# Optimization experiments

Measured on AMD Instinct MI355X. Metric: run time of the kernel, lower is better.

The kernel has to match this reference:

```python
import jax, jax.numpy as jnp
import numpy as np

Z1, COND, HID, NSTEP, B = 128, 12, 1024, 32, 4096


def setup_inputs() -> dict:
    key = jax.random.key(0)
    ks = jax.random.split(key, 10)
    s = 0.05  # init scale for learned params
    return {
        "z": jax.random.normal(ks[0], (B, Z1), jnp.float32),
        "condition": jax.random.uniform(ks[1], (B, NSTEP, COND), jnp.float32),
        "iteration": 1000,
        # nn.GRUCell params (gate order: r, z, n)
        "W_ih": jax.random.normal(ks[2], (3 * HID, Z1 + COND), jnp.float32) * s,
        "W_hh": jax.random.normal(ks[3], (3 * HID, HID), jnp.float32) * s,
        "b_ih": jax.random.normal(ks[4], (3 * HID,), jnp.float32) * s,
        "b_hh": jax.random.normal(ks[5], (3 * HID,), jnp.float32) * s,
        # linear_init_0
        "W_init": jax.random.normal(ks[6], (HID, Z1), jnp.float32) * s,
        "b_init": jax.random.normal(ks[7], (HID,), jnp.float32) * s,
        # linear_out_0
        "W_out": jax.random.normal(ks[8], (COND, HID), jnp.float32) * s,
        "b_out": jax.random.normal(ks[9], (COND,), jnp.float32) * s,
    }


def reference(z, condition, iteration, W_ih, W_hh, b_ih, b_hh, W_init, b_init, W_out, b_out):
    # Deterministic teacher-forcing path (training, eps=1): feedback at step i
    # is zeros for i=0, else condition[:, i-1, :]. iteration only affects the
    # stochastic eps schedule, which is dropped for determinism.
    del iteration
    b = z.shape[0]
    hx = jnp.tanh(z @ W_init.T + b_init)  # [B, H]
    feed = jnp.concatenate(
        [jnp.zeros((b, 1, COND), z.dtype), condition[:, :-1, :]], axis=1)  # [B, T, C]
    inputs = jnp.concatenate(
        [feed, jnp.broadcast_to(z[:, None, :], (b, NSTEP, z.shape[1]))], axis=-1)
    # precompute all input-to-hidden projections, time-major: [T, B, 3H]
    gi = jnp.einsum('bti,gi->tbg', inputs, W_ih) + b_ih

    def step(h, gi_t):
        gh = h @ W_hh.T + b_hh
        i_r, i_z, i_n = jnp.split(gi_t, 3, axis=-1)
        h_r, h_z, h_n = jnp.split(gh, 3, axis=-1)
        r = jax.nn.sigmoid(i_r + h_r)
        u = jax.nn.sigmoid(i_z + h_z)
        n = jnp.tanh(i_n + r * h_n)
        h_new = (1.0 - u) * n + u * h
        x = jax.nn.sigmoid(h_new @ W_out.T + b_out)  # [B, C]
        return h_new, x

    _, xs = jax.lax.scan(step, hx, gi)  # xs: [T, B, C]
    return jnp.transpose(xs, (1, 0, 2))  # [B, T, C]
```

## Files before the change

kernel.cpp:

```cpp
#include <hip/hip_runtime.h>
#include <stdint.h>

#define BB    4096
#define Z1D   128
#define CD    12
#define HD    1024
#define TT    32
#define N3H   3072
#define KAUG  1184
#define NGP   3168
#define NPH0B 1088
#define ACOLS 160

typedef __bf16 bf16;
typedef __bf16 bf16x2 __attribute__((ext_vector_type(2)));
typedef __bf16 bf16x8 __attribute__((ext_vector_type(8)));
typedef float  f32x4  __attribute__((ext_vector_type(4)));
typedef float  f4     __attribute__((ext_vector_type(4)));

typedef const __attribute__((address_space(1))) void* as1cv;
typedef __attribute__((address_space(3))) void* as3v;

__device__ __forceinline__ float sigm(float x){ return 1.0f/(1.0f+__expf(-x)); }
__device__ __forceinline__ float tanhfast(float x){ return 1.0f - 2.0f/(1.0f+__expf(2.0f*x)); }

__device__ __forceinline__ int rowOfN(int np, int& g){
  int jb = np/96; int r = np - jb*96; g = r>>5; int jl = r&31;
  return g*1024 + jb*32 + jl;
}

__global__ __launch_bounds__(256)
void prep_k(const float* __restrict__ z, const float* __restrict__ Wih,
            const float* __restrict__ Whh, const float* __restrict__ bih,
            const float* __restrict__ bhh, const float* __restrict__ Winit,
            const float* __restrict__ Wout,
            bf16* __restrict__ Wg, bf16* __restrict__ Wzn, bf16* __restrict__ Wi0,
            bf16* __restrict__ zbf, float* __restrict__ biasz,
            float* __restrict__ bhhn, float* __restrict__ bihn,
            bf16* __restrict__ A0, bf16* __restrict__ A1)
{
  const int N1 = NGP*KAUG;
  const int N2 = NPH0B*Z1D;
  const int N3 = NPH0B*Z1D;
  const int N4 = BB*Z1D;
  const int N5 = N3H;
  const int N6 = HD;
  const int N6b= HD;
  const int N7 = 2*BB*ACOLS;
  int idx = blockIdx.x*256 + threadIdx.x;
  if (idx < N1){
    int np = idx/KAUG, k = idx - np*KAUG;
    float v = 0.0f;
    if (np < N3H){
      int g; int row = rowOfN(np, g);
      if (k < 1024) v = Whh[(size_t)row*HD + k];
      else if (g < 2){
        if (k < 1036)      v = Wih[(size_t)row*140 + (k-1024)];
        else if (k < 1164) v = Wih[(size_t)row*140 + 12 + (k-1036)];
      }
    } else {
      int c = np - N3H;
      if (c < CD && k < 1024) v = Wout[(size_t)c*HD + k];
    }
    Wg[idx] = (bf16)v;
    return;
  }
  idx -= N1;
  if (idx < N2){
    int jn = idx/Z1D, kk = idx - jn*Z1D;
    Wzn[idx] = (jn < HD) ? (bf16)Wih[(size_t)(2048+jn)*140 + 12 + kk] : (bf16)0.0f;
    return;
  }
  idx -= N2;
  if (idx < N3){
    int jn = idx/Z1D, kk = idx - jn*Z1D;
    Wi0[idx] = (jn < HD) ? (bf16)Winit[(size_t)jn*Z1D + kk] : (bf16)0.0f;
    return;
  }
  idx -= N3;
  if (idx < N4){ zbf[idx] = (bf16)z[idx]; return; }
  idx -= N4;
  if (idx < N5){
    int g; int row = rowOfN(idx, g);
    biasz[idx] = (g < 2) ? (bih[row] + bhh[row]) : 0.0f;
    return;
  }
  idx -= N5;
  if (idx < N6){ bhhn[idx] = bhh[2048 + idx]; return; }
  idx -= N6;
  if (idx < N6b){ bihn[idx] = bih[2048 + idx]; return; }
  idx -= N6b;
  if (idx < N7){
    int j = (idx < BB*ACOLS) ? idx : idx - BB*ACOLS;
    int b = j / ACOLS, kk = j - b*ACOLS;
    int k = 1024 + kk;
    bf16 v = (bf16)0.0f;
    if (k >= 1036 && k < 1164) v = (bf16)z[(size_t)b*Z1D + (k-1036)];
    if (idx < BB*ACOLS) A0[(size_t)b*KAUG + k] = v;
    else                A1[(size_t)b*KAUG + k] = v;
  }
}

template<int EP>
__global__ __launch_bounds__(256, 5)
void gemm_k(const bf16* __restrict__ A, int lda,
            const bf16* __restrict__ Bw, int ldb, int ksteps,
            const bf16* __restrict__ zpn, bf16* __restrict__ zpnw,
            const float* __restrict__ biasz, const float* __restrict__ bias1,
            const float* __restrict__ bhhn,
            const float* __restrict__ Wih, const float* __restrict__ cond,
            const bf16* __restrict__ Acur, bf16* __restrict__ Anext,
            const float* __restrict__ bout, float* __restrict__ outg, int t)
{
  __shared__ bf16 lA[2][128*32];
  __shared__ bf16 lB[2][96*32];
  const int tid = threadIdx.x, wid = tid>>6, lane = tid&63;
  const int l15 = lane&15, l4 = lane>>4;

  int bx, by;
  if constexpr (EP == 2){
    int bid = blockIdx.x;
    int x = bid & 7, k = bid >> 3;
    bx = k >> 2;
    by = x*4 + (k & 3);
  } else {
    bx = blockIdx.x; by = blockIdx.y;
  }
  const int n0 = bx*96, m0 = by*128;

  f32x4 acc[2][6];
  #pragma unroll
  for (int i=0;i<2;++i)
    #pragma unroll
    for (int j=0;j<6;++j) acc[i][j] = (f32x4){0.f,0.f,0.f,0.f};

  auto STAGE = [&](int buf, int ks){
    const int k0 = ks*32;
    const bf16* gA = A + (size_t)m0*lda + k0;
    #pragma unroll
    for (int r=0; r<2; ++r){
      int q = r*256 + tid;
      int row = q>>2, slot = q&3;
      int sg = slot ^ ((row>>1)&3);
      const bf16* gp = gA + (size_t)row*lda + sg*8;
      bf16* lp = &lA[buf][(size_t)(r*256 + wid*64)*8];
      __builtin_amdgcn_global_load_lds((as1cv)gp, (as3v)lp, 16, 0, 0);
    }
    const bf16* gB = Bw + (size_t)n0*ldb + k0;
    {
      int q = tid;
      int row = q>>2, slot = q&3;
      int sg = slot ^ ((row>>1)&3);
      const bf16* gp = gB + (size_t)row*ldb + sg*8;
      bf16* lp = &lB[buf][(size_t)(wid*64)*8];
      __builtin_amdgcn_global_load_lds((as1cv)gp, (as3v)lp, 16, 0, 0);
    }
    if (tid < 128){
      int q = 256 + tid;
      int row = q>>2, slot = q&3;
      int sg = slot ^ ((row>>1)&3);
      const bf16* gp = gB + (size_t)row*ldb + sg*8;
      bf16* lp = &lB[buf][(size_t)(256 + wid*64)*8];
      __builtin_amdgcn_global_load_lds((as1cv)gp, (as3v)lp, 16, 0, 0);
    }
  };

  const int sl = (l4 ^ ((l15>>1)&3))*8;

  int cur = 0;
  STAGE(0, 0);
  for (int ks=0; ks<ksteps; ++ks){
    __syncthreads();
    if (ks+1 < ksteps) STAGE(cur^1, ks+1);
    bf16x8 af0 = *(const bf16x8*)&lA[cur][(wid*32 +  0 + l15)*32 + sl];
    bf16x8 af1 = *(const bf16x8*)&lA[cur][(wid*32 + 16 + l15)*32 + sl];
    #pragma unroll
    for (int cf=0; cf<6; ++cf){
      bf16x8 bfr = *(const bf16x8*)&lB[cur][(cf*16 + l15)*32 + sl];
      acc[0][cf] = __builtin_amdgcn_mfma_f32_16x16x32_bf16(af0, bfr, acc[0][cf], 0,0,0);
      acc[1][cf] = __builtin_amdgcn_mfma_f32_16x16x32_bf16(af1, bfr, acc[1][cf], 0,0,0);
    }
    cur ^= 1;
  }

  const int rbase = m0 + wid*32 + l4*4;

  if constexpr (EP == 0){
    #pragma unroll
    for (int rf=0; rf<2; ++rf)
      #pragma unroll
      for (int cf=0; cf<6; ++cf){
        int jn = n0 + cf*16 + l15;
        if (jn < HD){
          float bi = bias1[jn];
          #pragma unroll
          for (int reg=0; reg<4; ++reg){
            int b = rbase + rf*16 + reg;
            zpnw[(size_t)b*HD + jn] = (bf16)(acc[rf][cf][reg] + bi);
          }
        }
      }
  }
  else if constexpr (EP == 1){
    #pragma unroll
    for (int rf=0; rf<2; ++rf)
      #pragma unroll
      for (int cf=0; cf<6; ++cf){
        int jn = n0 + cf*16 + l15;
        if (jn < HD){
          float bi = bias1[jn];
          #pragma unroll
          for (int reg=0; reg<4; ++reg){
            int b = rbase + rf*16 + reg;
            Anext[(size_t)b*KAUG + jn] = (bf16)tanhfast(acc[rf][cf][reg] + bi);
          }
        }
      }
  }
  else if (bx == 32){
    if (t > 0){
      int c = l15;
      if (c < CD){
        float bo = bout[c];
        #pragma unroll
        for (int rf=0; rf<2; ++rf){
          #pragma unroll
          for (int reg=0; reg<4; ++reg){
            int b = rbase + rf*16 + reg;
            outg[((size_t)b*TT + (t-1))*CD + c] = sigm(acc[rf][0][reg] + bo);
          }
        }
      }
    }
  }
  else {
    const int jblk = bx;
    float wfn[2][12];
    #pragma unroll
    for (int jf=0; jf<2; ++jf){
      int jn = jblk*32 + jf*16 + l15;
      const f4* wr = (const f4*)(Wih + (size_t)(2048 + jn)*140);
      f4 w0 = wr[0], w1 = wr[1], w2 = wr[2];
      #pragma unroll
      for (int c=0;c<4;++c){ wfn[jf][c]=w0[c]; wfn[jf][4+c]=w1[c]; wfn[jf][8+c]=w2[c]; }
    }
    #pragma unroll
    for (int rf=0; rf<2; ++rf){
      #pragma unroll
      for (int reg=0; reg<4; ++reg){
        int b = rbase + rf*16 + reg;
        const bf16* fr = Acur + (size_t)b*KAUG + 1024;
        bf16x8 f8 = *(const bf16x8*)fr;
        float fd[12];
        #pragma unroll
        for (int c=0;c<8;++c) fd[c] = (float)f8[c];
        #pragma unroll
        for (int c=8;c<12;++c) fd[c] = (float)fr[c];
        #pragma unroll
        for (int jf=0; jf<2; ++jf){
          int jn = jblk*32 + jf*16 + l15;
          int np = n0 + jf*16 + l15;
          float aR = acc[rf][jf  ][reg] + biasz[np];
          float aZ = acc[rf][2+jf][reg] + biasz[np+32];
          float hN = acc[rf][4+jf][reg] + bhhn[jn];
          float iN = (float)zpn[(size_t)b*HD + jn];
          float fdot = 0.0f;
          #pragma unroll
          for (int c=0;c<12;++c) fdot += fd[c]*wfn[jf][c];
          float r = sigm(aR);
          float u = sigm(aZ);
          float nn = tanhfast(iN + fdot + r*hN);
          float hp = (float)Acur[(size_t)b*KAUG + jn];
          float hv = (1.0f-u)*nn + u*hp;
          Anext[(size_t)b*KAUG + jn] = (bf16)hv;
        }
      }
    }
    if (jblk == 0){
      for (int i = tid; i < 128*CD; i += 256){
        int rr = i/CD, c = i - rr*CD;
        int b = m0 + rr;
        Anext[(size_t)b*KAUG + 1024 + c] = (bf16)cond[((size_t)b*TT + t)*CD + c];
      }
    }
  }
}

__global__ __launch_bounds__(256)
void out_k(const bf16* __restrict__ hstate, const float* __restrict__ Wout,
           const float* __restrict__ bout, float* __restrict__ out, int t)
{
  __shared__ float sw[CD*HD];
  __shared__ float sb[CD];
  const int tid = threadIdx.x;
  for (int i=tid; i<CD*HD; i+=256) sw[i] = Wout[i];
  if (tid < CD) sb[tid] = bout[tid];
  __syncthreads();
  const int wid = tid>>6, lane = tid&63;
  const int b0 = blockIdx.x*8 + wid*2;
  for (int rr=0; rr<2; ++rr){
    int b = b0 + rr;
    const bf16* hr = hstate + (size_t)b*KAUG;
    float p[CD];
    #pragma unroll
    for (int c=0;c<CD;++c) p[c] = 0.0f;
    #pragma unroll
    for (int j=0;j<8;++j){
      int idx = lane*2 + j*128;
      bf16x2 hv = *(const bf16x2*)&hr[idx];
      float h0 = (float)hv[0], h1 = (float)hv[1];
      #pragma unroll
      for (int c=0;c<CD;++c) p[c] += h0*sw[c*HD + idx] + h1*sw[c*HD + idx + 1];
    }
    #pragma unroll
    for (int c=0;c<CD;++c){
      float v = p[c];
      #pragma unroll
      for (int m=32;m>=1;m>>=1) v += __shfl_xor(v, m, 64);
      if (lane == 0) out[((size_t)b*TT + t)*CD + c] = sigm(v + sb[c]);
    }
  }
}

extern "C" void kernel_launch(void* const* d_in, const int* in_sizes, int n_in,
                              void* d_out, int out_size, void* d_ws, size_t ws_size,
                              hipStream_t stream) {
  const float* z     = (const float*)d_in[0];
  const float* cond  = (const float*)d_in[1];
  const float* Wih   = (const float*)d_in[3];
  const float* Whh   = (const float*)d_in[4];
  const float* bih   = (const float*)d_in[5];
  const float* bhh   = (const float*)d_in[6];
  const float* Winit = (const float*)d_in[7];
  const float* binit = (const float*)d_in[8];
  const float* Wout  = (const float*)d_in[9];
  const float* bout  = (const float*)d_in[10];
  float* out = (float*)d_out;

  char* ws = (char*)d_ws;
  size_t off = 0;
  auto carve = [&](size_t bytes)->char*{
    char* p = ws + off; off += (bytes + 255) & ~(size_t)255; return p;
  };
  bf16*  Wg    = (bf16*) carve((size_t)NGP*KAUG*2);
  bf16*  Wzn   = (bf16*) carve((size_t)NPH0B*Z1D*2);
  bf16*  Wi0   = (bf16*) carve((size_t)NPH0B*Z1D*2);
  bf16*  zbf   = (bf16*) carve((size_t)BB*Z1D*2);
  float* biasz = (float*)carve((size_t)N3H*4);
  float* bhhn  = (float*)carve((size_t)HD*4);
  float* bihn  = (float*)carve((size_t)HD*4);
  bf16*  zpn   = (bf16*) carve((size_t)BB*HD*2);
  bf16*  A0    = (bf16*) carve((size_t)BB*KAUG*2);
  bf16*  A1    = (bf16*) carve((size_t)BB*KAUG*2);

  {
    long total = (long)NGP*KAUG + 2L*NPH0B*Z1D + (long)BB*Z1D + N3H + 2*HD
               + 2L*BB*ACOLS;
    int blocks = (int)((total + 255)/256);
    prep_k<<<blocks, 256, 0, stream>>>(z, Wih, Whh, bih, bhh, Winit, Wout,
                                       Wg, Wzn, Wi0, zbf, biasz, bhhn, bihn,
                                       A0, A1);
  }
  gemm_k<0><<<dim3(11,32), 256, 0, stream>>>(zbf, Z1D, Wzn, Z1D, 4,
      nullptr, zpn, nullptr, bihn, nullptr, nullptr, nullptr,
      nullptr, nullptr, nullptr, nullptr, 0);
  gemm_k<1><<<dim3(11,32), 256, 0, stream>>>(zbf, Z1D, Wi0, Z1D, 4,
      nullptr, nullptr, nullptr, binit, nullptr, nullptr, nullptr,
      nullptr, A0, nullptr, nullptr, 0);

  for (int t = 0; t < TT; ++t){
    const bf16* Ac = (t & 1) ? A1 : A0;
    bf16*       An = (t & 1) ? A0 : A1;
    gemm_k<2><<<1056, 256, 0, stream>>>(Ac, KAUG, Wg, KAUG, 37,
        zpn, nullptr, biasz, nullptr, bhhn, Wih, cond,
        Ac, An, bout, out, t);
  }
  out_k<<<512, 256, 0, stream>>>(A0, Wout, bout, out, 31);
}
```

Measured before the change: 1.915 ms.

## Use dedicated larger-tile GRU step kernel with 128x192 tiles and K=64 stages

Splits the per-timestep recurrent GEMM out of the generic gemm_k into a new gru_step kernel. Each block now computes a 128x192 tile with a 2x2 warp layout and 64-wide K stages, and the augmented K dimension is padded from 1184 to 1216 so it divides evenly. Larger tiles raise arithmetic intensity and halve the number of K iterations and barriers, which cuts LDS and global traffic per FLOP. In exchange it uses more registers and LDS per block (launch bounds of 2), so occupancy drops, and the grid shrinks to 544 blocks, which may leave some CUs underused.

```diff
diff --git a/kernel.cpp b/kernel.cpp
--- a/kernel.cpp
+++ b/kernel.cpp
@@ -7,10 +7,11 @@
 #define HD    1024
 #define TT    32
 #define N3H   3072
-#define KAUG  1184
-#define NGP   3168
+#define KAUG  1216
+#define NGP   3264
 #define NPH0B 1088
-#define ACOLS 160
+#define ACOLS 192
+#define KS64  19
 
 typedef __bf16 bf16;
 typedef __bf16 bf16x2 __attribute__((ext_vector_type(2)));
@@ -105,27 +106,14 @@
 __global__ __launch_bounds__(256, 5)
 void gemm_k(const bf16* __restrict__ A, int lda,
             const bf16* __restrict__ Bw, int ldb, int ksteps,
-            const bf16* __restrict__ zpn, bf16* __restrict__ zpnw,
-            const float* __restrict__ biasz, const float* __restrict__ bias1,
-            const float* __restrict__ bhhn,
-            const float* __restrict__ Wih, const float* __restrict__ cond,
-            const bf16* __restrict__ Acur, bf16* __restrict__ Anext,
-            const float* __restrict__ bout, float* __restrict__ outg, int t)
+            bf16* __restrict__ zpnw, const float* __restrict__ bias1,
+            bf16* __restrict__ Anext)
 {
   __shared__ bf16 lA[2][128*32];
   __shared__ bf16 lB[2][96*32];
   const int tid = threadIdx.x, wid = tid>>6, lane = tid&63;
   const int l15 = lane&15, l4 = lane>>4;
-
-  int bx, by;
-  if constexpr (EP == 2){
-    int bid = blockIdx.x;
-    int x = bid & 7, k = bid >> 3;
-    bx = k >> 2;
-    by = x*4 + (k & 3);
-  } else {
-    bx = blockIdx.x; by = blockIdx.y;
-  }
+  const int bx = blockIdx.x, by = blockIdx.y;
   const int n0 = bx*96, m0 = by*128;
 
   f32x4 acc[2][6];
@@ -166,7 +154,6 @@
   };
 
   const int sl = (l4 ^ ((l15>>1)&3))*8;
-
   int cur = 0;
   STAGE(0, 0);
   for (int ks=0; ks<ksteps; ++ks){
@@ -184,71 +171,132 @@
   }
 
   const int rbase = m0 + wid*32 + l4*4;
-
-  if constexpr (EP == 0){
-    #pragma unroll
-    for (int rf=0; rf<2; ++rf)
-      #pragma unroll
-      for (int cf=0; cf<6; ++cf){
-        int jn = n0 + cf*16 + l15;
-        if (jn < HD){
-          float bi = bias1[jn];
-          #pragma unroll
-          for (int reg=0; reg<4; ++reg){
-            int b = rbase + rf*16 + reg;
+  #pragma unroll
+  for (int rf=0; rf<2; ++rf)
+    #pragma unroll
+    for (int cf=0; cf<6; ++cf){
+      int jn = n0 + cf*16 + l15;
+      if (jn < HD){
+        float bi = bias1[jn];
+        #pragma unroll
+        for (int reg=0; reg<4; ++reg){
+          int b = rbase + rf*16 + reg;
+          if constexpr (EP == 0)
             zpnw[(size_t)b*HD + jn] = (bf16)(acc[rf][cf][reg] + bi);
-          }
+          else
+            Anext[(size_t)b*KAUG + jn] = (bf16)tanhfast(acc[rf][cf][reg] + bi);
         }
       }
-  }
-  else if constexpr (EP == 1){
-    #pragma unroll
-    for (int rf=0; rf<2; ++rf)
-      #pragma unroll
-      for (int cf=0; cf<6; ++cf){
-        int jn = n0 + cf*16 + l15;
-        if (jn < HD){
-          float bi = bias1[jn];
-          #pragma unroll
-          for (int reg=0; reg<4; ++reg){
-            int b = rbase + rf*16 + reg;
-            Anext[(size_t)b*KAUG + jn] = (bf16)tanhfast(acc[rf][cf][reg] + bi);
-          }
+    }
+}
+
+__global__ __launch_bounds__(256, 2)
+void gru_step(const bf16* __restrict__ Acur, const bf16* __restrict__ Wg,
+              const bf16* __restrict__ zpn, const float* __restrict__ biasz,
+              const float* __restrict__ bhhn, const float* __restrict__ Wih,
+              const float* __restrict__ cond, bf16* __restrict__ Anext,
+              const float* __restrict__ bout, float* __restrict__ outg, int t)
+{
+  __shared__ bf16 lA[2][128*64];
+  __shared__ bf16 lB[2][192*64];
+  const int tid = threadIdx.x, wid = tid>>6, lane = tid&63;
+  const int l15 = lane&15, l4 = lane>>4;
+  const int wm = wid>>1, wn = wid&1;
+
+  const int bid = blockIdx.x;
+  const int x = bid & 7, k = bid >> 3;
+  const int bx = k >> 2;
+  const int by = x*4 + (k & 3);
+  const int n0 = bx*192, m0 = by*128;
+
+  f32x4 acc[4][6];
+  #pragma unroll
+  for (int i=0;i<4;++i)
+    #pragma unroll
+    for (int j=0;j<6;++j) acc[i][j] = (f32x4){0.f,0.f,0.f,0.f};
+
+  auto STAGE = [&](int buf, int ks){
+    const int k0 = ks*64;
+    const bf16* gA = Acur + (size_t)m0*KAUG + k0;
+    #pragma unroll
+    for (int r=0; r<4; ++r){
+      int q = r*256 + tid;
+      int row = q>>3, slot = q&7;
+      int sg = slot ^ (row&7);
+      const bf16* gp = gA + (size_t)row*KAUG + sg*8;
+      bf16* lp = &lA[buf][(size_t)(r*256 + wid*64)*8];
+      __builtin_amdgcn_global_load_lds((as1cv)gp, (as3v)lp, 16, 0, 0);
+    }
+    const bf16* gB = Wg + (size_t)n0*KAUG + k0;
+    #pragma unroll
+    for (int r=0; r<6; ++r){
+      int q = r*256 + tid;
+      int row = q>>3, slot = q&7;
+      int sg = slot ^ (row&7);
+      const bf16* gp = gB + (size_t)row*KAUG + sg*8;
+      bf16* lp = &lB[buf][(size_t)(r*256 + wid*64)*8];
+      __builtin_amdgcn_global_load_lds((as1cv)gp, (as3v)lp, 16, 0, 0);
+    }
+  };
+
+  int cur = 0;
+  STAGE(0, 0);
+  for (int ks=0; ks<KS64; ++ks){
+    __syncthreads();
+    if (ks+1 < KS64) STAGE(cur^1, ks+1);
+    #pragma unroll
+    for (int kk=0; kk<2; ++kk){
+      bf16x8 af[4];
+      #pragma unroll
+      for (int mf=0; mf<4; ++mf){
+        int row = wm*64 + mf*16 + l15;
+        int sp = (kk*4 + l4) ^ (row&7);
+        af[mf] = *(const bf16x8*)&lA[cur][row*64 + sp*8];
+      }
+      #pragma unroll
+      for (int nf=0; nf<6; ++nf){
+        int row = wn*96 + nf*16 + l15;
+        int sp = (kk*4 + l4) ^ (row&7);
+        bf16x8 bfr = *(const bf16x8*)&lB[cur][row*64 + sp*8];
+        acc[0][nf] = __builtin_amdgcn_mfma_f32_16x16x32_bf16(af[0], bfr, acc[0][nf], 0,0,0);
+        acc[1][nf] = __builtin_amdgcn_mfma_f32_16x16x32_bf16(af[1], bfr, acc[1][nf], 0,0,0);
+        acc[2][nf] = __builtin_amdgcn_mfma_f32_16x16x32_bf16(af[2], bfr, acc[2][nf], 0,0,0);
+        acc[3][nf] = __builtin_amdgcn_mfma_f32_16x16x32_bf16(af[3], bfr, acc[3][nf], 0,0,0);
+      }
+    }
+    cur ^= 1;
+  }
+
+  const int rbase = m0 + wm*64 + l4*4;
+
+  if (bx == 16){
+    if (wn == 0 && t > 0 && l15 < CD){
+      float bo = bout[l15];
+      #pragma unroll
+      for (int mf=0; mf<4; ++mf){
+        #pragma unroll
+        for (int reg=0; reg<4; ++reg){
+          int b = rbase + mf*16 + reg;
+          outg[((size_t)b*TT + (t-1))*CD + l15] = sigm(acc[mf][0][reg] + bo);
         }
       }
-  }
-  else if (bx == 32){
-    if (t > 0){
-      int c = l15;
-      if (c < CD){
-        float bo = bout[c];
-        #pragma unroll
-        for (int rf=0; rf<2; ++rf){
-          #pragma unroll
-          for (int reg=0; reg<4; ++reg){
-            int b = rbase + rf*16 + reg;
-            outg[((size_t)b*TT + (t-1))*CD + c] = sigm(acc[rf][0][reg] + bo);
-          }
-        }
-      }
-    }
-  }
-  else {
-    const int jblk = bx;
+    }
+  } else {
+    const int jg = bx*2 + wn;
     float wfn[2][12];
     #pragma unroll
     for (int jf=0; jf<2; ++jf){
-      int jn = jblk*32 + jf*16 + l15;
+      int jn = jg*32 + jf*16 + l15;
       const f4* wr = (const f4*)(Wih + (size_t)(2048 + jn)*140);
       f4 w0 = wr[0], w1 = wr[1], w2 = wr[2];
       #pragma unroll
       for (int c=0;c<4;++c){ wfn[jf][c]=w0[c]; wfn[jf][4+c]=w1[c]; wfn[jf][8+c]=w2[c]; }
     }
     #pragma unroll
-    for (int rf=0; rf<2; ++rf){
+    for (int mf=0; mf<4; ++mf){
       #pragma unroll
       for (int reg=0; reg<4; ++reg){
-        int b = rbase + rf*16 + reg;
+        int b = rbase + mf*16 + reg;
         const bf16* fr = Acur + (size_t)b*KAUG + 1024;
         bf16x8 f8 = *(const bf16x8*)fr;
         float fd[12];
@@ -258,11 +306,11 @@
         for (int c=8;c<12;++c) fd[c] = (float)fr[c];
         #pragma unroll
         for (int jf=0; jf<2; ++jf){
-          int jn = jblk*32 + jf*16 + l15;
-          int np = n0 + jf*16 + l15;
-          float aR = acc[rf][jf  ][reg] + biasz[np];
-          float aZ = acc[rf][2+jf][reg] + biasz[np+32];
-          float hN = acc[rf][4+jf][reg] + bhhn[jn];
+          int jn = jg*32 + jf*16 + l15;
+          int np = jg*96 + jf*16 + l15;
+          float aR = acc[mf][jf  ][reg] + biasz[np];
+          float aZ = acc[mf][2+jf][reg] + biasz[np+32];
+          float hN = acc[mf][4+jf][reg] + bhhn[jn];
           float iN = (float)zpn[(size_t)b*HD + jn];
           float fdot = 0.0f;
           #pragma unroll
@@ -276,7 +324,7 @@
         }
       }
     }
-    if (jblk == 0){
+    if (bx == 0){
       for (int i = tid; i < 128*CD; i += 256){
         int rr = i/CD, c = i - rr*CD;
         int b = m0 + rr;
@@ -362,18 +410,15 @@
                                        A0, A1);
   }
   gemm_k<0><<<dim3(11,32), 256, 0, stream>>>(zbf, Z1D, Wzn, Z1D, 4,
-      nullptr, zpn, nullptr, bihn, nullptr, nullptr, nullptr,
-      nullptr, nullptr, nullptr, nullptr, 0);
+      zpn, bihn, nullptr);
   gemm_k<1><<<dim3(11,32), 256, 0, stream>>>(zbf, Z1D, Wi0, Z1D, 4,
-      nullptr, nullptr, nullptr, binit, nullptr, nullptr, nullptr,
-      nullptr, A0, nullptr, nullptr, 0);
+      nullptr, binit, A0);
 
   for (int t = 0; t < TT; ++t){
     const bf16* Ac = (t & 1) ? A1 : A0;
     bf16*       An = (t & 1) ? A0 : A1;
-    gemm_k<2><<<1056, 256, 0, stream>>>(Ac, KAUG, Wg, KAUG, 37,
-        zpn, nullptr, biasz, nullptr, bhhn, Wih, cond,
-        Ac, An, bout, out, t);
+    gru_step<<<544, 256, 0, stream>>>(Ac, Wg, zpn, biasz, bhhn, Wih, cond,
+                                      An, bout, out, t);
   }
   out_k<<<512, 256, 0, stream>>>(A0, Wout, bout, out, 31);
 }
```

Measured after the change: 1.839 ms. 4.0% less time.
